# Optimization experiments

Hardware: AMD Instinct MI355X
Metric: run time of the kernel (lower is better)

The kernel has to match this reference:

```python
import jax, jax.numpy as jnp
import numpy as np

N_NODES = 50000
N_EDGES = 800000
D_NODE = 64
D_EDGE = 64
D_OUT = 64
D_HID = 128
LN_EPS = 1e-5


def _mlp_params(key, d_in):
    # layer sizes: [d_in, D_HID, D_HID, D_OUT]; weights stored [in, out]
    ks = jax.random.split(key, 3)
    dims = [d_in, D_HID, D_HID, D_OUT]
    params = []
    for i in range(3):
        s = 1.0 / np.sqrt(dims[i])
        params.append(jax.random.uniform(ks[i], (dims[i], dims[i + 1]), minval=-s, maxval=s, dtype=jnp.float32))
        params.append(jnp.zeros((dims[i + 1],), jnp.float32))
    # LayerNorm gamma/beta
    params.append(jnp.ones((D_OUT,), jnp.float32))
    params.append(jnp.zeros((D_OUT,), jnp.float32))
    return params


def _mlp_ln(h, W0, b0, W1, b1, W2, b2, g, beta):
    h = jax.nn.relu(h @ W0 + b0)
    h = jax.nn.relu(h @ W1 + b1)
    h = h @ W2 + b2
    mu = jnp.mean(h, axis=-1, keepdims=True)
    var = jnp.mean(jnp.square(h - mu), axis=-1, keepdims=True)
    return (h - mu) * jax.lax.rsqrt(var + LN_EPS) * g + beta


def setup_inputs() -> dict:
    key = jax.random.key(0)
    k = jax.random.split(key, 8)
    inp = {
        "x": jax.random.normal(k[0], (N_NODES, D_NODE), jnp.float32),
        "mesh_edge_index": jax.random.randint(k[1], (2, N_EDGES), 0, N_NODES, dtype=jnp.int32),
        "mesh_edge_attr": jax.random.normal(k[2], (N_EDGES, D_EDGE), jnp.float32),
        "world_edge_index": jax.random.randint(k[3], (2, N_EDGES), 0, N_NODES, dtype=jnp.int32),
        "world_edge_attr": jax.random.normal(k[4], (N_EDGES, D_EDGE), jnp.float32),
    }
    names = ["W0", "b0", "W1", "b1", "W2", "b2", "ln_g", "ln_b"]
    for pref, kk, d_in in [("mesh", k[5], 2 * D_NODE + D_EDGE),
                           ("world", k[6], 2 * D_NODE + D_EDGE),
                           ("upd", k[7], D_NODE + 2 * D_OUT)]:
        ps = _mlp_params(kk, d_in)
        for nm, p in zip(names, ps):
            inp[f"{pref}_{nm}"] = p
    return inp


def _edge_block(x, edge_index, edge_attr, W0, b0, W1, b1, W2, b2, g, beta):
    src, dst = edge_index[0], edge_index[1]  # PyG: x_j = source, x_i = target
    x_i = x[dst]  # [E, D_NODE]
    x_j = x[src]
    concat = jnp.concatenate([x_i, x_j, edge_attr], axis=-1)  # [E, 2D+De]
    new_edge = edge_attr + _mlp_ln(concat, W0, b0, W1, b1, W2, b2, g, beta)
    agg = jax.ops.segment_sum(new_edge, dst, num_segments=N_NODES)  # 'add' aggr at target
    return agg, new_edge


def reference(x, mesh_edge_index, mesh_edge_attr, world_edge_index, world_edge_attr,
              mesh_W0, mesh_b0, mesh_W1, mesh_b1, mesh_W2, mesh_b2, mesh_ln_g, mesh_ln_b,
              world_W0, world_b0, world_W1, world_b1, world_W2, world_b2, world_ln_g, world_ln_b,
              upd_W0, upd_b0, upd_W1, upd_b1, upd_W2, upd_b2, upd_ln_g, upd_ln_b):
    agg_m, new_edge_m = _edge_block(x, mesh_edge_index, mesh_edge_attr,
                                    mesh_W0, mesh_b0, mesh_W1, mesh_b1, mesh_W2, mesh_b2, mesh_ln_g, mesh_ln_b)
    agg_w, new_edge_w = _edge_block(x, world_edge_index, world_edge_attr,
                                    world_W0, world_b0, world_W1, world_b1, world_W2, world_b2, world_ln_g, world_ln_b)
    concat = jnp.concatenate([x, agg_m, agg_w], axis=-1)  # [N, D_NODE + 2*D_OUT]
    x_new = x + _mlp_ln(concat, upd_W0, upd_b0, upd_W1, upd_b1, upd_W2, upd_b2, upd_ln_g, upd_ln_b)
    return x_new, new_edge_m, new_edge_w
```

## Files before the change

kernel.cpp:

```cpp
#include <hip/hip_runtime.h>


#define NNODES 50000
#define NEDGES 800000
#define NBLK 512
#define NCHUNK 196

typedef __bf16 bf16x8 __attribute__((ext_vector_type(8)));
typedef float f32x4 __attribute__((ext_vector_type(4)));
#define MFMA(a, b, c) __builtin_amdgcn_mfma_f32_16x16x32_bf16(a, b, c, 0, 0, 0)

#define OFF_A 0
#define OFF_H0 24576
#define OFF_P 40960
#define OFF_PAR 43008
#define SMEM 44800

__device__ __forceinline__ unsigned short f2bf(float f) {
  unsigned u = __builtin_bit_cast(unsigned, f);
  u = (u + 0x7fffu + ((u >> 16) & 1u)) >> 16;
  return (unsigned short)u;
}
__device__ __forceinline__ unsigned long long pk4(f32x4 v) {
  union { unsigned short h[4]; unsigned long long u; } p;
  p.h[0] = f2bf(v[0]); p.h[1] = f2bf(v[1]); p.h[2] = f2bf(v[2]); p.h[3] = f2bf(v[3]);
  return p.u;
}
__device__ __forceinline__ int4 pk8(float4 a, float4 b) {
  union { unsigned short us[8]; int4 v; } u;
  u.us[0] = f2bf(a.x); u.us[1] = f2bf(a.y); u.us[2] = f2bf(a.z); u.us[3] = f2bf(a.w);
  u.us[4] = f2bf(b.x); u.us[5] = f2bf(b.y); u.us[6] = f2bf(b.z); u.us[7] = f2bf(b.w);
  return u.v;
}
__device__ __forceinline__ int4 ldpk(const float* p) {
  return pk8(*(const float4*)p, *(const float4*)(p + 4));
}

template <bool EDGE>
__global__ __launch_bounds__(512, 4) void mlp_block(
    const float* __restrict__ g1, const float* __restrict__ g2,
    const float* __restrict__ g3, const unsigned short* __restrict__ xb,
    const int* __restrict__ srcI, const int* __restrict__ dstI,
    const unsigned short* __restrict__ Wt,
    const float* __restrict__ b0, const float* __restrict__ b1,
    const float* __restrict__ b2, const float* __restrict__ gam,
    const float* __restrict__ bet, float* __restrict__ outp, int M) {
  __shared__ __align__(16) char sm[SMEM];
  const int tid = threadIdx.x, lane = tid & 63, wave = tid >> 6;
  const int lrow = lane & 15, cg = lane >> 4;
  const unsigned short* Wt0 = Wt;
  const unsigned short* Wt1 = Wt + 24576;
  const unsigned short* Wt2 = Wt + 40960;
  const int ntiles = (M + 63) >> 6;
  const int cg2 = wave & 3, rg = wave >> 2;

  for (int i = tid; i < 448; i += 512) {
    float v;
    if (i < 128) v = b0[i];
    else if (i < 256) v = b1[i - 128];
    else if (i < 320) v = b2[i - 256];
    else if (i < 384) v = gam[i - 320];
    else v = bet[i - 384];
    ((float*)(sm + OFF_PAR))[i] = v;
  }
  const float* PAR = (const float*)(sm + OFF_PAR);

  bf16x8 w0f[6], w1f[4], w2f[4];
#pragma unroll
  for (int kk = 0; kk < 6; ++kk)
    w0f[kk] = *(const bf16x8*)(Wt0 + (wave * 16 + lrow) * 192 + kk * 32 + cg * 8);
#pragma unroll
  for (int kk = 0; kk < 4; ++kk)
    w1f[kk] = *(const bf16x8*)(Wt1 + (wave * 16 + lrow) * 128 + kk * 32 + cg * 8);
#pragma unroll
  for (int kk = 0; kk < 4; ++kk)
    w2f[kk] = *(const bf16x8*)(Wt2 + (cg2 * 16 + lrow) * 128 + kk * 32 + cg * 8);

  const int srow = (tid >> 5) * 4 + ((tid & 31) >> 3), oct = tid & 7;

  int4 pxd, pxs, pat;
  auto LOADT = [&](int tt) {
    const int row = tt * 64 + srow;
    if (EDGE) {
      const int d = dstI[row], s2 = srcI[row];
      pxd = *(const int4*)(xb + (size_t)d * 64 + oct * 8);
      pxs = *(const int4*)(xb + (size_t)s2 * 64 + oct * 8);
      pat = ldpk(g3 + (size_t)row * 64 + oct * 8);
    } else {
      const int rr = min(row, M - 1);
      pxd = ldpk(g1 + (size_t)rr * 64 + oct * 8);
      pxs = ldpk(g2 + (size_t)rr * 64 + oct * 8);
      pat = ldpk(g3 + (size_t)rr * 64 + oct * 8);
    }
  };
  auto STAGE = [&]() {
    char* a0 = sm + OFF_A + srow * 384;
    const int swz = (srow & 7) << 4;
    *(int4*)(a0 + ((oct * 16) ^ swz)) = pxd;
    *(int4*)(a0 + ((128 + oct * 16) ^ swz)) = pxs;
    *(int4*)(a0 + ((256 + oct * 16) ^ swz)) = pat;
  };

  int t = blockIdx.x;
  if (t >= ntiles) return;
  LOADT(t);
  STAGE();

  for (; t < ntiles; t += NBLK) {
    const int tn = t + NBLK;
    const bool more = tn < ntiles;
    __syncthreads();
    if (more) LOADT(tn);
    {
      const f32x4 bb0 = *(const f32x4*)(PAR + wave * 16 + cg * 4);
#pragma unroll
      for (int rt = 0; rt < 4; ++rt) {
        const int row = rt * 16 + lrow, swz = (row & 7) << 4;
        const char* ab = sm + OFF_A + row * 384;
        f32x4 acc = {0.f, 0.f, 0.f, 0.f};
#pragma unroll
        for (int kk = 0; kk < 6; ++kk)
          acc = MFMA(w0f[kk], *(const bf16x8*)(ab + ((kk * 64 + cg * 16) ^ swz)), acc);
        f32x4 h;
#pragma unroll
        for (int q = 0; q < 4; ++q) h[q] = fmaxf(acc[q] + bb0[q], 0.f);
        *(unsigned long long*)(sm + OFF_H0 + row * 256 + ((wave * 32 + cg * 8) ^ swz)) = pk4(h);
      }
    }
    __syncthreads();
    {
      const f32x4 bb1 = *(const f32x4*)(PAR + 128 + wave * 16 + cg * 4);
#pragma unroll
      for (int rt = 0; rt < 4; ++rt) {
        const int row = rt * 16 + lrow, swz = (row & 7) << 4;
        const char* hb = sm + OFF_H0 + row * 256;
        f32x4 acc = {0.f, 0.f, 0.f, 0.f};
#pragma unroll
        for (int kk = 0; kk < 4; ++kk)
          acc = MFMA(w1f[kk], *(const bf16x8*)(hb + ((kk * 64 + cg * 16) ^ swz)), acc);
        f32x4 h;
#pragma unroll
        for (int q = 0; q < 4; ++q) h[q] = fmaxf(acc[q] + bb1[q], 0.f);
        *(unsigned long long*)(sm + OFF_A + row * 384 + ((wave * 32 + cg * 8) ^ swz)) = pk4(h);
      }
    }
    __syncthreads();
    f32x4 accE[2];
    {
      const f32x4 bb2 = *(const f32x4*)(PAR + 256 + cg2 * 16 + cg * 4);
#pragma unroll
      for (int j = 0; j < 2; ++j) {
        const int row = (rg * 2 + j) * 16 + lrow, swz = (row & 7) << 4;
        const char* hb = sm + OFF_A + row * 384;
        f32x4 acc = {0.f, 0.f, 0.f, 0.f};
#pragma unroll
        for (int kk = 0; kk < 4; ++kk)
          acc = MFMA(w2f[kk], *(const bf16x8*)(hb + ((kk * 64 + cg * 16) ^ swz)), acc);
#pragma unroll
        for (int q = 0; q < 4; ++q) acc[q] += bb2[q];
        float s = acc[0] + acc[1] + acc[2] + acc[3];
        float ss = acc[0] * acc[0] + acc[1] * acc[1] + acc[2] * acc[2] + acc[3] * acc[3];
        s += __shfl_xor(s, 16, 64); s += __shfl_xor(s, 32, 64);
        ss += __shfl_xor(ss, 16, 64); ss += __shfl_xor(ss, 32, 64);
        if (cg == 0) *(float2*)(sm + OFF_P + row * 32 + cg2 * 8) = make_float2(s, ss);
        accE[j] = acc;
      }
    }
    __syncthreads();
    {
      const f32x4 gv = *(const f32x4*)(PAR + 320 + cg2 * 16 + cg * 4);
      const f32x4 bv = *(const f32x4*)(PAR + 384 + cg2 * 16 + cg * 4);
#pragma unroll
      for (int j = 0; j < 2; ++j) {
        const int row = (rg * 2 + j) * 16 + lrow, gr = t * 64 + row;
        float4 p0 = *(const float4*)(sm + OFF_P + row * 32);
        float4 p1 = *(const float4*)(sm + OFF_P + row * 32 + 16);
        float s = p0.x + p0.z + p1.x + p1.z, ss = p0.y + p0.w + p1.y + p1.w;
        float mean = s * (1.f / 64.f);
        float var = fmaxf(ss * (1.f / 64.f) - mean * mean, 0.f);
        float inv = rsqrtf(var + 1e-5f);
        const int col = cg2 * 16 + cg * 4;
        const int grc = EDGE ? gr : min(gr, M - 1);
        const f32x4 r = *(const f32x4*)(g3 + (size_t)grc * 64 + col);
        f32x4 av = accE[j], o;
#pragma unroll
        for (int q = 0; q < 4; ++q) o[q] = (av[q] - mean) * inv * gv[q] + bv[q] + r[q];
        if (EDGE || gr < M) *(f32x4*)(outp + (size_t)gr * 64 + col) = o;
      }
    }
    if (more) STAGE();
  }
}

__global__ __launch_bounds__(256) void agg_k(const float* __restrict__ em,
                                             const float* __restrict__ ew,
                                             const int* __restrict__ permM,
                                             const int* __restrict__ permW,
                                             const int* __restrict__ rpM,
                                             const int* __restrict__ rpW,
                                             float* __restrict__ aggm,
                                             float* __restrict__ aggw) {
  const int lane = threadIdx.x & 63;
  const int r4 = lane >> 4, cq = lane & 15;
  const int w = (blockIdx.x * 256 + threadIdx.x) >> 6;
  const int nw = gridDim.x * 4;
  for (int dd = w; dd < 2 * NNODES; dd += nw) {
    const bool s1 = dd >= NNODES;
    const int d = s1 ? dd - NNODES : dd;
    const float* oute = s1 ? ew : em;
    const int* perm = s1 ? permW : permM;
    const int* rp = s1 ? rpW : rpM;
    const int s = rp[d], e = rp[d + 1];
    f32x4 acc = {0.f, 0.f, 0.f, 0.f}, acc2 = {0.f, 0.f, 0.f, 0.f};
    int j = s + r4;
    for (; j + 4 < e; j += 8) {
      const int ra = perm[j], rb = perm[j + 4];
      const f32x4 va = *(const f32x4*)(oute + (size_t)ra * 64 + cq * 4);
      const f32x4 vb = *(const f32x4*)(oute + (size_t)rb * 64 + cq * 4);
#pragma unroll
      for (int q = 0; q < 4; ++q) { acc[q] += va[q]; acc2[q] += vb[q]; }
    }
    if (j < e) {
      const int ra = perm[j];
      const f32x4 va = *(const f32x4*)(oute + (size_t)ra * 64 + cq * 4);
#pragma unroll
      for (int q = 0; q < 4; ++q) acc[q] += va[q];
    }
#pragma unroll
    for (int q = 0; q < 4; ++q) {
      acc[q] += acc2[q];
      acc[q] += __shfl_xor(acc[q], 16, 64);
      acc[q] += __shfl_xor(acc[q], 32, 64);
    }
    float* agg = s1 ? aggw : aggm;
    if (r4 == 0) *(f32x4*)(agg + (size_t)d * 64 + cq * 4) = acc;
  }
}

struct PrepArgs { const float* w[9]; unsigned short* wt[3]; };

__global__ void prep_w(PrepArgs pa) {
  int i = blockIdx.x * 256 + threadIdx.x;
  if (i >= 3 * 49152) return;
  int mlp = i / 49152;
  int rem = i - mlp * 49152;
  int mat, off, K, N;
  if (rem < 24576)      { mat = 0; off = 0;     K = 192; N = 128; }
  else if (rem < 40960) { mat = 1; off = 24576; K = 128; N = 128; }
  else                  { mat = 2; off = 40960; K = 128; N = 64;  }
  int local = rem - off;
  int n = local / K, k = local - n * K;
  if (mlp == 2 && mat == 0) k = (k + 64) % 192;
  pa.wt[mlp][rem] = f2bf(pa.w[mlp * 3 + mat][k * N + n]);
}

__global__ void prep_x(const float* __restrict__ x, unsigned short* __restrict__ xb) {
  int i = blockIdx.x * 256 + threadIdx.x;
  if (i < NNODES * 8) *(int4*)(xb + (size_t)i * 8) = ldpk(x + (size_t)i * 8);
}

__global__ void zero_f4(float4* p, int n) {
  int i = blockIdx.x * blockDim.x + threadIdx.x;
  if (i < n) p[i] = make_float4(0.f, 0.f, 0.f, 0.f);
}

__global__ void hist_k(const int* __restrict__ dM, const int* __restrict__ dW,
                       int* __restrict__ curM, int* __restrict__ curW, int E) {
  int i = blockIdx.x * 256 + threadIdx.x;
  if (i < E) {
    atomicAdd(curM + dM[i], 1);
    atomicAdd(curW + dW[i], 1);
  }
}

__global__ __launch_bounds__(64) void csum_k(const int* __restrict__ curM,
                                             const int* __restrict__ curW,
                                             int* __restrict__ csum) {
  const int c = blockIdx.x, set = c >= NCHUNK, c0 = c - set * NCHUNK;
  const int* cnt = set ? curW : curM;
  const int lane = threadIdx.x;
  const int base = c0 * 256 + lane * 4;
  int s = 0;
  if (base + 3 < NNODES) {
    int4 v = *(const int4*)(cnt + base);
    s = v.x + v.y + v.z + v.w;
  } else {
    for (int k = 0; k < 4; ++k) if (base + k < NNODES) s += cnt[base + k];
  }
#pragma unroll
  for (int off = 1; off < 64; off <<= 1) s += __shfl_xor(s, off, 64);
  if (lane == 0) csum[c] = s;
}

__global__ __launch_bounds__(512) void cscan_k(const int* __restrict__ csum,
                                               int* __restrict__ cbase) {
  __shared__ int buf[512];
  const int tid = threadIdx.x;
  buf[tid] = (tid < 2 * NCHUNK) ? csum[tid] : 0;
  __syncthreads();
  for (int off = 1; off < 512; off <<= 1) {
    int nv = (tid >= off) ? buf[tid - off] : 0;
    __syncthreads();
    buf[tid] += nv;
    __syncthreads();
  }
  if (tid < 2 * NCHUNK) {
    const int set = tid >= NCHUNK;
    int excl = tid ? buf[tid - 1] : 0;
    if (set) excl -= buf[NCHUNK - 1];
    cbase[tid] = excl;
  }
}

__global__ __launch_bounds__(64) void rp_k(int* __restrict__ curM, int* __restrict__ curW,
                                           const int* __restrict__ cbase,
                                           int* __restrict__ rpM, int* __restrict__ rpW) {
  const int c = blockIdx.x, set = c >= NCHUNK, c0 = c - set * NCHUNK;
  int* cnt = set ? curW : curM;
  int* rp = set ? rpW : rpM;
  const int lane = threadIdx.x;
  const int idx = c0 * 256 + lane * 4;
  int v[4];
#pragma unroll
  for (int k = 0; k < 4; ++k) v[k] = (idx + k < NNODES) ? cnt[idx + k] : 0;
  const int ls = v[0] + v[1] + v[2] + v[3];
  int ex = ls;
#pragma unroll
  for (int off = 1; off < 64; off <<= 1) {
    int nv = __shfl_up(ex, off, 64);
    if (lane >= off) ex += nv;
  }
  int run = cbase[c] + (ex - ls);
#pragma unroll
  for (int k = 0; k < 4; ++k) {
    if (idx + k < NNODES) {
      rp[idx + k] = run;
      cnt[idx + k] = run;
      run += v[k];
    }
  }
  if (c0 == 0 && lane == 0) rp[NNODES] = NEDGES;
}

__global__ void scatter_k(const int* __restrict__ dM, const int* __restrict__ dW,
                          int* __restrict__ curM, int* __restrict__ curW,
                          int* __restrict__ permM, int* __restrict__ permW, int E) {
  int i = blockIdx.x * 256 + threadIdx.x;
  if (i < E) {
    int p = atomicAdd(curM + dM[i], 1);
    permM[p] = i;
    p = atomicAdd(curW + dW[i], 1);
    permW[p] = i;
  }
}

extern "C" void kernel_launch(void* const* d_in, const int* in_sizes, int n_in,
                              void* d_out, int out_size, void* d_ws, size_t ws_size,
                              hipStream_t stream) {
  const float* x      = (const float*)d_in[0];
  const int*   meIdx  = (const int*)d_in[1];
  const float* meAttr = (const float*)d_in[2];
  const int*   weIdx  = (const int*)d_in[3];
  const float* weAttr = (const float*)d_in[4];

  float* out_x  = (float*)d_out;
  float* out_em = out_x + (size_t)NNODES * 64;
  float* out_ew = out_em + (size_t)NEDGES * 64;

  char* ws = (char*)d_ws;
  unsigned short* WtM = (unsigned short*)ws;
  unsigned short* WtW = (unsigned short*)(ws + 98304);
  unsigned short* WtU = (unsigned short*)(ws + 196608);
  unsigned short* xb  = (unsigned short*)(ws + 294912);
  float* aggm = (float*)(ws + 6694912);
  float* aggw = (float*)(ws + 19494912);
  char* p = ws + 32294912;
  int* curM  = (int*)p;
  int* curW  = curM + NNODES;
  int* rpM   = (int*)(p + 400000);
  int* rpW   = rpM + 50016;
  int* permM = rpW + 50016;
  int* permW = permM + NEDGES;
  int* csum  = permW + NEDGES;
  int* cbase = csum + 512;

  zero_f4<<<dim3(98), dim3(256), 0, stream>>>((float4*)curM, 25000);

  PrepArgs pa;
  for (int m = 0; m < 3; ++m)
    for (int l = 0; l < 3; ++l)
      pa.w[m * 3 + l] = (const float*)d_in[5 + m * 8 + l * 2];
  pa.wt[0] = WtM; pa.wt[1] = WtW; pa.wt[2] = WtU;
  prep_w<<<dim3(576), dim3(256), 0, stream>>>(pa);
  prep_x<<<dim3(1563), dim3(256), 0, stream>>>(x, xb);

  hist_k<<<dim3(3125), dim3(256), 0, stream>>>(meIdx + NEDGES, weIdx + NEDGES, curM, curW, NEDGES);
  csum_k<<<dim3(2 * NCHUNK), dim3(64), 0, stream>>>(curM, curW, csum);
  cscan_k<<<dim3(1), dim3(512), 0, stream>>>(csum, cbase);
  rp_k<<<dim3(2 * NCHUNK), dim3(64), 0, stream>>>(curM, curW, cbase, rpM, rpW);
  scatter_k<<<dim3(3125), dim3(256), 0, stream>>>(meIdx + NEDGES, weIdx + NEDGES,
                                                  curM, curW, permM, permW, NEDGES);

  mlp_block<true><<<dim3(NBLK), dim3(512), 0, stream>>>(
      nullptr, nullptr, meAttr, xb, meIdx, meIdx + NEDGES, WtM,
      (const float*)d_in[6], (const float*)d_in[8], (const float*)d_in[10],
      (const float*)d_in[11], (const float*)d_in[12],
      out_em, NEDGES);
  mlp_block<true><<<dim3(NBLK), dim3(512), 0, stream>>>(
      nullptr, nullptr, weAttr, xb, weIdx, weIdx + NEDGES, WtW,
      (const float*)d_in[14], (const float*)d_in[16], (const float*)d_in[18],
      (const float*)d_in[19], (const float*)d_in[20],
      out_ew, NEDGES);

  agg_k<<<dim3(4096), dim3(256), 0, stream>>>(out_em, out_ew, permM, permW, rpM, rpW, aggm, aggw);

  mlp_block<false><<<dim3(NBLK), dim3(512), 0, stream>>>(
      aggm, aggw, x, nullptr, nullptr, nullptr, WtU,
      (const float*)d_in[22], (const float*)d_in[24], (const float*)d_in[26],
      (const float*)d_in[27], (const float*)d_in[28],
      out_x, NNODES);
}
```

Measured before the change: 750.3 us.

## Merge mesh/world edge MLP launches and gather bf16 edge copies in aggregation

The two edge-block MLP launches become one grid of twice the blocks, with each half selecting its own edge set, weights and parameters. This removes a launch and the tail of the first kernel. When the workspace is large enough, the edge MLP also writes a bf16 copy of each new edge feature. The aggregation kernel then gathers those bf16 rows instead of fp32 rows, halving the bytes of the random gather at the cost of an extra streaming write and bf16 rounding in the segment sums.

```diff
diff --git a/kernel.cpp b/kernel.cpp
--- a/kernel.cpp
+++ b/kernel.cpp
@@ -21,6 +21,9 @@
   u = (u + 0x7fffu + ((u >> 16) & 1u)) >> 16;
   return (unsigned short)u;
 }
+__device__ __forceinline__ float bf2f(unsigned short h) {
+  return __builtin_bit_cast(float, (unsigned)h << 16);
+}
 __device__ __forceinline__ unsigned long long pk4(f32x4 v) {
   union { unsigned short h[4]; unsigned long long u; } p;
   p.h[0] = f2bf(v[0]); p.h[1] = f2bf(v[1]); p.h[2] = f2bf(v[2]); p.h[3] = f2bf(v[3]);
@@ -35,17 +38,44 @@
 __device__ __forceinline__ int4 ldpk(const float* p) {
   return pk8(*(const float4*)p, *(const float4*)(p + 4));
 }
+__device__ __forceinline__ f32x4 ub4(uint2 p) {
+  f32x4 r;
+  r[0] = bf2f((unsigned short)p.x); r[1] = bf2f((unsigned short)(p.x >> 16));
+  r[2] = bf2f((unsigned short)p.y); r[3] = bf2f((unsigned short)(p.y >> 16));
+  return r;
+}
 
 template <bool EDGE>
 __global__ __launch_bounds__(512, 4) void mlp_block(
     const float* __restrict__ g1, const float* __restrict__ g2,
-    const float* __restrict__ g3, const unsigned short* __restrict__ xb,
-    const int* __restrict__ srcI, const int* __restrict__ dstI,
-    const unsigned short* __restrict__ Wt,
-    const float* __restrict__ b0, const float* __restrict__ b1,
-    const float* __restrict__ b2, const float* __restrict__ gam,
-    const float* __restrict__ bet, float* __restrict__ outp, int M) {
+    const float* __restrict__ g3A, const float* __restrict__ g3B,
+    const unsigned short* __restrict__ xb,
+    const int* __restrict__ srcA, const int* __restrict__ dstA,
+    const int* __restrict__ srcB, const int* __restrict__ dstB,
+    const unsigned short* __restrict__ WtA,
+    const float* __restrict__ b0A, const float* __restrict__ b1A,
+    const float* __restrict__ b2A, const float* __restrict__ gmA,
+    const float* __restrict__ btA,
+    const float* __restrict__ b0B, const float* __restrict__ b1B,
+    const float* __restrict__ b2B, const float* __restrict__ gmB,
+    const float* __restrict__ btB,
+    float* __restrict__ outA, unsigned short* __restrict__ oebA, int M) {
   __shared__ __align__(16) char sm[SMEM];
+  const int gstr = EDGE ? (gridDim.x >> 1) : gridDim.x;
+  const int set = EDGE ? (int)(blockIdx.x >= (unsigned)gstr) : 0;
+  const int bid0 = blockIdx.x - set * gstr;
+  const float* g3 = set ? g3B : g3A;
+  const int* srcI = set ? srcB : srcA;
+  const int* dstI = set ? dstB : dstA;
+  const unsigned short* Wt = WtA + set * 49152;
+  const float* b0 = set ? b0B : b0A;
+  const float* b1 = set ? b1B : b1A;
+  const float* b2 = set ? b2B : b2A;
+  const float* gam = set ? gmB : gmA;
+  const float* bet = set ? btB : btA;
+  float* outp = outA + (size_t)set * NEDGES * 64;
+  unsigned short* oeb = oebA ? oebA + (size_t)set * NEDGES * 64 : nullptr;
+
   const int tid = threadIdx.x, lane = tid & 63, wave = tid >> 6;
   const int lrow = lane & 15, cg = lane >> 4;
   const unsigned short* Wt0 = Wt;
@@ -101,13 +131,13 @@
     *(int4*)(a0 + ((256 + oct * 16) ^ swz)) = pat;
   };
 
-  int t = blockIdx.x;
+  int t = bid0;
   if (t >= ntiles) return;
   LOADT(t);
   STAGE();
 
-  for (; t < ntiles; t += NBLK) {
-    const int tn = t + NBLK;
+  for (; t < ntiles; t += gstr) {
+    const int tn = t + gstr;
     const bool more = tn < ntiles;
     __syncthreads();
     if (more) LOADT(tn);
@@ -186,6 +216,7 @@
 #pragma unroll
         for (int q = 0; q < 4; ++q) o[q] = (av[q] - mean) * inv * gv[q] + bv[q] + r[q];
         if (EDGE || gr < M) *(f32x4*)(outp + (size_t)gr * 64 + col) = o;
+        if (EDGE && oeb) *(unsigned long long*)(oeb + (size_t)gr * 64 + col) = pk4(o);
       }
     }
     if (more) STAGE();
@@ -194,6 +225,7 @@
 
 __global__ __launch_bounds__(256) void agg_k(const float* __restrict__ em,
                                              const float* __restrict__ ew,
+                                             const unsigned short* __restrict__ oeb,
                                              const int* __restrict__ permM,
                                              const int* __restrict__ permW,
                                              const int* __restrict__ rpM,
@@ -207,24 +239,39 @@
   for (int dd = w; dd < 2 * NNODES; dd += nw) {
     const bool s1 = dd >= NNODES;
     const int d = s1 ? dd - NNODES : dd;
-    const float* oute = s1 ? ew : em;
     const int* perm = s1 ? permW : permM;
     const int* rp = s1 ? rpW : rpM;
     const int s = rp[d], e = rp[d + 1];
     f32x4 acc = {0.f, 0.f, 0.f, 0.f}, acc2 = {0.f, 0.f, 0.f, 0.f};
     int j = s + r4;
-    for (; j + 4 < e; j += 8) {
-      const int ra = perm[j], rb = perm[j + 4];
-      const f32x4 va = *(const f32x4*)(oute + (size_t)ra * 64 + cq * 4);
-      const f32x4 vb = *(const f32x4*)(oute + (size_t)rb * 64 + cq * 4);
-#pragma unroll
-      for (int q = 0; q < 4; ++q) { acc[q] += va[q]; acc2[q] += vb[q]; }
-    }
-    if (j < e) {
-      const int ra = perm[j];
-      const f32x4 va = *(const f32x4*)(oute + (size_t)ra * 64 + cq * 4);
-#pragma unroll
-      for (int q = 0; q < 4; ++q) acc[q] += va[q];
+    if (oeb) {
+      const unsigned short* ob = oeb + (size_t)(s1 ? NEDGES : 0) * 64;
+      for (; j + 4 < e; j += 8) {
+        const int ra = perm[j], rb = perm[j + 4];
+        const f32x4 va = ub4(*(const uint2*)(ob + (size_t)ra * 64 + cq * 4));
+        const f32x4 vb = ub4(*(const uint2*)(ob + (size_t)rb * 64 + cq * 4));
+#pragma unroll
+        for (int q = 0; q < 4; ++q) { acc[q] += va[q]; acc2[q] += vb[q]; }
+      }
+      if (j < e) {
+        const f32x4 va = ub4(*(const uint2*)(ob + (size_t)perm[j] * 64 + cq * 4));
+#pragma unroll
+        for (int q = 0; q < 4; ++q) acc[q] += va[q];
+      }
+    } else {
+      const float* oute = s1 ? ew : em;
+      for (; j + 4 < e; j += 8) {
+        const int ra = perm[j], rb = perm[j + 4];
+        const f32x4 va = *(const f32x4*)(oute + (size_t)ra * 64 + cq * 4);
+        const f32x4 vb = *(const f32x4*)(oute + (size_t)rb * 64 + cq * 4);
+#pragma unroll
+        for (int q = 0; q < 4; ++q) { acc[q] += va[q]; acc2[q] += vb[q]; }
+      }
+      if (j < e) {
+        const f32x4 va = *(const f32x4*)(oute + (size_t)perm[j] * 64 + cq * 4);
+#pragma unroll
+        for (int q = 0; q < 4; ++q) acc[q] += va[q];
+      }
     }
 #pragma unroll
     for (int q = 0; q < 4; ++q) {
@@ -369,7 +416,6 @@
 
   char* ws = (char*)d_ws;
   unsigned short* WtM = (unsigned short*)ws;
-  unsigned short* WtW = (unsigned short*)(ws + 98304);
   unsigned short* WtU = (unsigned short*)(ws + 196608);
   unsigned short* xb  = (unsigned short*)(ws + 294912);
   float* aggm = (float*)(ws + 6694912);
@@ -383,6 +429,10 @@
   int* permW = permM + NEDGES;
   int* csum  = permW + NEDGES;
   int* cbase = csum + 512;
+  char* pend = (char*)(cbase + 512);
+  const size_t oeb_bytes = (size_t)2 * NEDGES * 64 * 2;
+  unsigned short* oeb =
+      (ws_size >= (size_t)(pend - ws) + oeb_bytes) ? (unsigned short*)pend : nullptr;
 
   zero_f4<<<dim3(98), dim3(256), 0, stream>>>((float4*)curM, 25000);
 
@@ -390,7 +440,7 @@
   for (int m = 0; m < 3; ++m)
     for (int l = 0; l < 3; ++l)
       pa.w[m * 3 + l] = (const float*)d_in[5 + m * 8 + l * 2];
-  pa.wt[0] = WtM; pa.wt[1] = WtW; pa.wt[2] = WtU;
+  pa.wt[0] = WtM; pa.wt[1] = WtM + 49152; pa.wt[2] = WtU;
   prep_w<<<dim3(576), dim3(256), 0, stream>>>(pa);
   prep_x<<<dim3(1563), dim3(256), 0, stream>>>(x, xb);
 
@@ -401,22 +451,23 @@
   scatter_k<<<dim3(3125), dim3(256), 0, stream>>>(meIdx + NEDGES, weIdx + NEDGES,
                                                   curM, curW, permM, permW, NEDGES);
 
-  mlp_block<true><<<dim3(NBLK), dim3(512), 0, stream>>>(
-      nullptr, nullptr, meAttr, xb, meIdx, meIdx + NEDGES, WtM,
+  mlp_block<true><<<dim3(2 * NBLK), dim3(512), 0, stream>>>(
+      nullptr, nullptr, meAttr, weAttr, xb,
+      meIdx, meIdx + NEDGES, weIdx, weIdx + NEDGES, WtM,
       (const float*)d_in[6], (const float*)d_in[8], (const float*)d_in[10],
       (const float*)d_in[11], (const float*)d_in[12],
-      out_em, NEDGES);
-  mlp_block<true><<<dim3(NBLK), dim3(512), 0, stream>>>(
-      nullptr, nullptr, weAttr, xb, weIdx, weIdx + NEDGES, WtW,
       (const float*)d_in[14], (const float*)d_in[16], (const float*)d_in[18],
       (const float*)d_in[19], (const float*)d_in[20],
-      out_ew, NEDGES);
-
-  agg_k<<<dim3(4096), dim3(256), 0, stream>>>(out_em, out_ew, permM, permW, rpM, rpW, aggm, aggw);
+      out_em, oeb, NEDGES);
+
+  agg_k<<<dim3(4096), dim3(256), 0, stream>>>(out_em, out_ew, oeb,
+                                              permM, permW, rpM, rpW, aggm, aggw);
 
   mlp_block<false><<<dim3(NBLK), dim3(512), 0, stream>>>(
-      aggm, aggw, x, nullptr, nullptr, nullptr, WtU,
+      aggm, aggw, x, nullptr, xb,
+      nullptr, nullptr, nullptr, nullptr, WtU,
       (const float*)d_in[22], (const float*)d_in[24], (const float*)d_in[26],
       (const float*)d_in[27], (const float*)d_in[28],
-      out_x, NNODES);
-}
+      nullptr, nullptr, nullptr, nullptr, nullptr,
+      out_x, nullptr, NNODES);
+}
```

Measured after the change: 887.9 us. 1.18x slower.

## Process edges in destination-sorted order and aggregate from a contiguous bf16 copy

Applied to the files above, without the earlier changes.

The scatter kernel now also writes destination-sorted src and dst index arrays, and the edge MLP iterates edges in that sorted order. It gathers edge_attr and writes the fp32 output through the permutation. When the workspace is large enough, the edge kernel also writes a bf16 copy of each new edge row in sorted order. The aggregation kernel then streams that copy contiguously instead of doing permuted fp32 gathers. This trades scattered attr reads and output writes plus an extra bf16 store for contiguous aggregation reads and better node-feature locality, and adds bf16 rounding to the aggregated sums.

```diff
diff --git a/kernel.cpp b/kernel.cpp
--- a/kernel.cpp
+++ b/kernel.cpp
@@ -21,6 +21,9 @@
   u = (u + 0x7fffu + ((u >> 16) & 1u)) >> 16;
   return (unsigned short)u;
 }
+__device__ __forceinline__ float bf2f(unsigned short h) {
+  return __builtin_bit_cast(float, (unsigned)h << 16);
+}
 __device__ __forceinline__ unsigned long long pk4(f32x4 v) {
   union { unsigned short h[4]; unsigned long long u; } p;
   p.h[0] = f2bf(v[0]); p.h[1] = f2bf(v[1]); p.h[2] = f2bf(v[2]); p.h[3] = f2bf(v[3]);
@@ -35,16 +38,23 @@
 __device__ __forceinline__ int4 ldpk(const float* p) {
   return pk8(*(const float4*)p, *(const float4*)(p + 4));
 }
+__device__ __forceinline__ f32x4 ub4(uint2 p) {
+  f32x4 r;
+  r[0] = bf2f((unsigned short)p.x); r[1] = bf2f((unsigned short)(p.x >> 16));
+  r[2] = bf2f((unsigned short)p.y); r[3] = bf2f((unsigned short)(p.y >> 16));
+  return r;
+}
 
 template <bool EDGE>
 __global__ __launch_bounds__(512, 4) void mlp_block(
     const float* __restrict__ g1, const float* __restrict__ g2,
     const float* __restrict__ g3, const unsigned short* __restrict__ xb,
-    const int* __restrict__ srcI, const int* __restrict__ dstI,
-    const unsigned short* __restrict__ Wt,
+    const int* __restrict__ srcS, const int* __restrict__ dstS,
+    const int* __restrict__ perm, const unsigned short* __restrict__ Wt,
     const float* __restrict__ b0, const float* __restrict__ b1,
     const float* __restrict__ b2, const float* __restrict__ gam,
-    const float* __restrict__ bet, float* __restrict__ outp, int M) {
+    const float* __restrict__ bet, float* __restrict__ outp,
+    unsigned short* __restrict__ oebS, int M) {
   __shared__ __align__(16) char sm[SMEM];
   const int tid = threadIdx.x, lane = tid & 63, wave = tid >> 6;
   const int lrow = lane & 15, cg = lane >> 4;
@@ -82,10 +92,10 @@
   auto LOADT = [&](int tt) {
     const int row = tt * 64 + srow;
     if (EDGE) {
-      const int d = dstI[row], s2 = srcI[row];
+      const int d = dstS[row], s2 = srcS[row], e = perm[row];
       pxd = *(const int4*)(xb + (size_t)d * 64 + oct * 8);
       pxs = *(const int4*)(xb + (size_t)s2 * 64 + oct * 8);
-      pat = ldpk(g3 + (size_t)row * 64 + oct * 8);
+      pat = ldpk(g3 + (size_t)e * 64 + oct * 8);
     } else {
       const int rr = min(row, M - 1);
       pxd = ldpk(g1 + (size_t)rr * 64 + oct * 8);
@@ -180,12 +190,22 @@
         float var = fmaxf(ss * (1.f / 64.f) - mean * mean, 0.f);
         float inv = rsqrtf(var + 1e-5f);
         const int col = cg2 * 16 + cg * 4;
-        const int grc = EDGE ? gr : min(gr, M - 1);
-        const f32x4 r = *(const f32x4*)(g3 + (size_t)grc * 64 + col);
-        f32x4 av = accE[j], o;
-#pragma unroll
-        for (int q = 0; q < 4; ++q) o[q] = (av[q] - mean) * inv * gv[q] + bv[q] + r[q];
-        if (EDGE || gr < M) *(f32x4*)(outp + (size_t)gr * 64 + col) = o;
+        if (EDGE) {
+          const int pm = perm[gr];
+          const f32x4 r = *(const f32x4*)(g3 + (size_t)pm * 64 + col);
+          f32x4 av = accE[j], o;
+#pragma unroll
+          for (int q = 0; q < 4; ++q) o[q] = (av[q] - mean) * inv * gv[q] + bv[q] + r[q];
+          *(f32x4*)(outp + (size_t)pm * 64 + col) = o;
+          if (oebS) *(unsigned long long*)(oebS + (size_t)gr * 64 + col) = pk4(o);
+        } else {
+          const int grc = min(gr, M - 1);
+          const f32x4 r = *(const f32x4*)(g3 + (size_t)grc * 64 + col);
+          f32x4 av = accE[j], o;
+#pragma unroll
+          for (int q = 0; q < 4; ++q) o[q] = (av[q] - mean) * inv * gv[q] + bv[q] + r[q];
+          if (gr < M) *(f32x4*)(outp + (size_t)gr * 64 + col) = o;
+        }
       }
     }
     if (more) STAGE();
@@ -194,6 +214,7 @@
 
 __global__ __launch_bounds__(256) void agg_k(const float* __restrict__ em,
                                              const float* __restrict__ ew,
+                                             const unsigned short* __restrict__ oebS,
                                              const int* __restrict__ permM,
                                              const int* __restrict__ permW,
                                              const int* __restrict__ rpM,
@@ -207,24 +228,38 @@
   for (int dd = w; dd < 2 * NNODES; dd += nw) {
     const bool s1 = dd >= NNODES;
     const int d = s1 ? dd - NNODES : dd;
-    const float* oute = s1 ? ew : em;
-    const int* perm = s1 ? permW : permM;
     const int* rp = s1 ? rpW : rpM;
     const int s = rp[d], e = rp[d + 1];
     f32x4 acc = {0.f, 0.f, 0.f, 0.f}, acc2 = {0.f, 0.f, 0.f, 0.f};
     int j = s + r4;
-    for (; j + 4 < e; j += 8) {
-      const int ra = perm[j], rb = perm[j + 4];
-      const f32x4 va = *(const f32x4*)(oute + (size_t)ra * 64 + cq * 4);
-      const f32x4 vb = *(const f32x4*)(oute + (size_t)rb * 64 + cq * 4);
-#pragma unroll
-      for (int q = 0; q < 4; ++q) { acc[q] += va[q]; acc2[q] += vb[q]; }
-    }
-    if (j < e) {
-      const int ra = perm[j];
-      const f32x4 va = *(const f32x4*)(oute + (size_t)ra * 64 + cq * 4);
-#pragma unroll
-      for (int q = 0; q < 4; ++q) acc[q] += va[q];
+    if (oebS) {
+      const unsigned short* ob = oebS + (size_t)(s1 ? NEDGES : 0) * 64;
+      for (; j + 4 < e; j += 8) {
+        const f32x4 va = ub4(*(const uint2*)(ob + (size_t)j * 64 + cq * 4));
+        const f32x4 vb = ub4(*(const uint2*)(ob + (size_t)(j + 4) * 64 + cq * 4));
+#pragma unroll
+        for (int q = 0; q < 4; ++q) { acc[q] += va[q]; acc2[q] += vb[q]; }
+      }
+      if (j < e) {
+        const f32x4 va = ub4(*(const uint2*)(ob + (size_t)j * 64 + cq * 4));
+#pragma unroll
+        for (int q = 0; q < 4; ++q) acc[q] += va[q];
+      }
+    } else {
+      const float* oute = s1 ? ew : em;
+      const int* perm = s1 ? permW : permM;
+      for (; j + 4 < e; j += 8) {
+        const int ra = perm[j], rb = perm[j + 4];
+        const f32x4 va = *(const f32x4*)(oute + (size_t)ra * 64 + cq * 4);
+        const f32x4 vb = *(const f32x4*)(oute + (size_t)rb * 64 + cq * 4);
+#pragma unroll
+        for (int q = 0; q < 4; ++q) { acc[q] += va[q]; acc2[q] += vb[q]; }
+      }
+      if (j < e) {
+        const f32x4 va = *(const f32x4*)(oute + (size_t)perm[j] * 64 + cq * 4);
+#pragma unroll
+        for (int q = 0; q < 4; ++q) acc[q] += va[q];
+      }
     }
 #pragma unroll
     for (int q = 0; q < 4; ++q) {
@@ -343,14 +378,19 @@
 }
 
 __global__ void scatter_k(const int* __restrict__ dM, const int* __restrict__ dW,
+                          const int* __restrict__ sM, const int* __restrict__ sW,
                           int* __restrict__ curM, int* __restrict__ curW,
-                          int* __restrict__ permM, int* __restrict__ permW, int E) {
+                          int* __restrict__ permM, int* __restrict__ permW,
+                          int* __restrict__ dstSM, int* __restrict__ dstSW,
+                          int* __restrict__ srcSM, int* __restrict__ srcSW, int E) {
   int i = blockIdx.x * 256 + threadIdx.x;
   if (i < E) {
-    int p = atomicAdd(curM + dM[i], 1);
-    permM[p] = i;
-    p = atomicAdd(curW + dW[i], 1);
-    permW[p] = i;
+    int d = dM[i];
+    int p = atomicAdd(curM + d, 1);
+    permM[p] = i; dstSM[p] = d; srcSM[p] = sM[i];
+    d = dW[i];
+    p = atomicAdd(curW + d, 1);
+    permW[p] = i; dstSW[p] = d; srcSW[p] = sW[i];
   }
 }
 
@@ -381,8 +421,16 @@
   int* rpW   = rpM + 50016;
   int* permM = rpW + 50016;
   int* permW = permM + NEDGES;
-  int* csum  = permW + NEDGES;
+  int* dstSM = permW + NEDGES;
+  int* dstSW = dstSM + NEDGES;
+  int* srcSM = dstSW + NEDGES;
+  int* srcSW = srcSM + NEDGES;
+  int* csum  = srcSW + NEDGES;
   int* cbase = csum + 512;
+  char* pend = (char*)(cbase + 512);
+  const size_t oeb_bytes = (size_t)2 * NEDGES * 64 * 2;
+  unsigned short* oebS =
+      (ws_size >= (size_t)(pend - ws) + oeb_bytes) ? (unsigned short*)pend : nullptr;
 
   zero_f4<<<dim3(98), dim3(256), 0, stream>>>((float4*)curM, 25000);
 
@@ -399,24 +447,27 @@
   cscan_k<<<dim3(1), dim3(512), 0, stream>>>(csum, cbase);
   rp_k<<<dim3(2 * NCHUNK), dim3(64), 0, stream>>>(curM, curW, cbase, rpM, rpW);
   scatter_k<<<dim3(3125), dim3(256), 0, stream>>>(meIdx + NEDGES, weIdx + NEDGES,
-                                                  curM, curW, permM, permW, NEDGES);
+                                                  meIdx, weIdx, curM, curW,
+                                                  permM, permW, dstSM, dstSW,
+                                                  srcSM, srcSW, NEDGES);
 
   mlp_block<true><<<dim3(NBLK), dim3(512), 0, stream>>>(
-      nullptr, nullptr, meAttr, xb, meIdx, meIdx + NEDGES, WtM,
+      nullptr, nullptr, meAttr, xb, srcSM, dstSM, permM, WtM,
       (const float*)d_in[6], (const float*)d_in[8], (const float*)d_in[10],
       (const float*)d_in[11], (const float*)d_in[12],
-      out_em, NEDGES);
+      out_em, oebS, NEDGES);
   mlp_block<true><<<dim3(NBLK), dim3(512), 0, stream>>>(
-      nullptr, nullptr, weAttr, xb, weIdx, weIdx + NEDGES, WtW,
+      nullptr, nullptr, weAttr, xb, srcSW, dstSW, permW, WtW,
       (const float*)d_in[14], (const float*)d_in[16], (const float*)d_in[18],
       (const float*)d_in[19], (const float*)d_in[20],
-      out_ew, NEDGES);
-
-  agg_k<<<dim3(4096), dim3(256), 0, stream>>>(out_em, out_ew, permM, permW, rpM, rpW, aggm, aggw);
+      out_ew, oebS ? oebS + (size_t)NEDGES * 64 : nullptr, NEDGES);
+
+  agg_k<<<dim3(4096), dim3(256), 0, stream>>>(out_em, out_ew, oebS,
+                                              permM, permW, rpM, rpW, aggm, aggw);
 
   mlp_block<false><<<dim3(NBLK), dim3(512), 0, stream>>>(
-      aggm, aggw, x, nullptr, nullptr, nullptr, WtU,
+      aggm, aggw, x, nullptr, nullptr, nullptr, nullptr, WtU,
       (const float*)d_in[22], (const float*)d_in[24], (const float*)d_in[26],
       (const float*)d_in[27], (const float*)d_in[28],
-      out_x, NNODES);
-}
+      out_x, nullptr, NNODES);
+}
```

Result: slower. 826.5 us (+10.2%).

## Fuse CSR edge aggregation into node update MLP kernel

Applied to the files above, without the earlier changes.

Removes the separate aggregation kernel and its fp32 aggm/aggw round trip through global memory. A new node_mlp kernel gathers each node's incoming mesh and world edge rows via the CSR permutation, sums them in registers, packs them to bf16 in shared memory, and runs the update MLP and LayerNorm directly. The grid is 782 blocks, one 64-row tile each, so the gather for a tile is serialized per thread (8 floats per thread, one row per 8 threads). The tile's MFMA work cannot start until its gather finishes, and the gather has less parallelism than the old agg_k.

```diff
diff --git a/kernel.cpp b/kernel.cpp
--- a/kernel.cpp
+++ b/kernel.cpp
@@ -34,6 +34,9 @@
 }
 __device__ __forceinline__ int4 ldpk(const float* p) {
   return pk8(*(const float4*)p, *(const float4*)(p + 4));
+}
+__device__ __forceinline__ void add4(float4& a, float4 v) {
+  a.x += v.x; a.y += v.y; a.z += v.z; a.w += v.w;
 }
 
 template <bool EDGE>
@@ -192,48 +195,166 @@
   }
 }
 
-__global__ __launch_bounds__(256) void agg_k(const float* __restrict__ em,
-                                             const float* __restrict__ ew,
-                                             const int* __restrict__ permM,
-                                             const int* __restrict__ permW,
-                                             const int* __restrict__ rpM,
-                                             const int* __restrict__ rpW,
-                                             float* __restrict__ aggm,
-                                             float* __restrict__ aggw) {
-  const int lane = threadIdx.x & 63;
-  const int r4 = lane >> 4, cq = lane & 15;
-  const int w = (blockIdx.x * 256 + threadIdx.x) >> 6;
-  const int nw = gridDim.x * 4;
-  for (int dd = w; dd < 2 * NNODES; dd += nw) {
-    const bool s1 = dd >= NNODES;
-    const int d = s1 ? dd - NNODES : dd;
-    const float* oute = s1 ? ew : em;
-    const int* perm = s1 ? permW : permM;
-    const int* rp = s1 ? rpW : rpM;
-    const int s = rp[d], e = rp[d + 1];
-    f32x4 acc = {0.f, 0.f, 0.f, 0.f}, acc2 = {0.f, 0.f, 0.f, 0.f};
-    int j = s + r4;
-    for (; j + 4 < e; j += 8) {
-      const int ra = perm[j], rb = perm[j + 4];
-      const f32x4 va = *(const f32x4*)(oute + (size_t)ra * 64 + cq * 4);
-      const f32x4 vb = *(const f32x4*)(oute + (size_t)rb * 64 + cq * 4);
-#pragma unroll
-      for (int q = 0; q < 4; ++q) { acc[q] += va[q]; acc2[q] += vb[q]; }
-    }
-    if (j < e) {
-      const int ra = perm[j];
-      const f32x4 va = *(const f32x4*)(oute + (size_t)ra * 64 + cq * 4);
-#pragma unroll
-      for (int q = 0; q < 4; ++q) acc[q] += va[q];
-    }
-#pragma unroll
-    for (int q = 0; q < 4; ++q) {
-      acc[q] += acc2[q];
-      acc[q] += __shfl_xor(acc[q], 16, 64);
-      acc[q] += __shfl_xor(acc[q], 32, 64);
-    }
-    float* agg = s1 ? aggw : aggm;
-    if (r4 == 0) *(f32x4*)(agg + (size_t)d * 64 + cq * 4) = acc;
+__global__ __launch_bounds__(512, 4) void node_mlp(
+    const float* __restrict__ xg, const float* __restrict__ em,
+    const float* __restrict__ ew, const int* __restrict__ permM,
+    const int* __restrict__ permW, const int* __restrict__ rpM,
+    const int* __restrict__ rpW, const unsigned short* __restrict__ Wt,
+    const float* __restrict__ b0, const float* __restrict__ b1,
+    const float* __restrict__ b2, const float* __restrict__ gam,
+    const float* __restrict__ bet, float* __restrict__ outp, int M) {
+  __shared__ __align__(16) char sm[SMEM];
+  const int tid = threadIdx.x, lane = tid & 63, wave = tid >> 6;
+  const int lrow = lane & 15, cg = lane >> 4;
+  const unsigned short* Wt0 = Wt;
+  const unsigned short* Wt1 = Wt + 24576;
+  const unsigned short* Wt2 = Wt + 40960;
+  const int ntiles = (M + 63) >> 6;
+  const int cg2 = wave & 3, rg = wave >> 2;
+
+  for (int i = tid; i < 448; i += 512) {
+    float v;
+    if (i < 128) v = b0[i];
+    else if (i < 256) v = b1[i - 128];
+    else if (i < 320) v = b2[i - 256];
+    else if (i < 384) v = gam[i - 320];
+    else v = bet[i - 384];
+    ((float*)(sm + OFF_PAR))[i] = v;
+  }
+  const float* PAR = (const float*)(sm + OFF_PAR);
+
+  bf16x8 w0f[6], w1f[4], w2f[4];
+#pragma unroll
+  for (int kk = 0; kk < 6; ++kk)
+    w0f[kk] = *(const bf16x8*)(Wt0 + (wave * 16 + lrow) * 192 + kk * 32 + cg * 8);
+#pragma unroll
+  for (int kk = 0; kk < 4; ++kk)
+    w1f[kk] = *(const bf16x8*)(Wt1 + (wave * 16 + lrow) * 128 + kk * 32 + cg * 8);
+#pragma unroll
+  for (int kk = 0; kk < 4; ++kk)
+    w2f[kk] = *(const bf16x8*)(Wt2 + (cg2 * 16 + lrow) * 128 + kk * 32 + cg * 8);
+
+  const int srow = (tid >> 5) * 4 + ((tid & 31) >> 3), oct = tid & 7;
+
+  for (int t = blockIdx.x; t < ntiles; t += gridDim.x) {
+    {
+      const int gr = t * 64 + srow;
+      const int rr = min(gr, M - 1);
+      const int4 px = ldpk(xg + (size_t)rr * 64 + oct * 8);
+      float4 am0 = {0.f, 0.f, 0.f, 0.f}, am1 = {0.f, 0.f, 0.f, 0.f};
+      float4 aw0 = {0.f, 0.f, 0.f, 0.f}, aw1 = {0.f, 0.f, 0.f, 0.f};
+      if (gr < M) {
+        int j = rpM[gr];
+        const int e = rpM[gr + 1];
+        for (; j + 1 < e; j += 2) {
+          const int pa = permM[j], pb = permM[j + 1];
+          const float* ra = em + (size_t)pa * 64 + oct * 8;
+          const float* rb = em + (size_t)pb * 64 + oct * 8;
+          add4(am0, *(const float4*)ra); add4(am1, *(const float4*)(ra + 4));
+          add4(am0, *(const float4*)rb); add4(am1, *(const float4*)(rb + 4));
+        }
+        if (j < e) {
+          const float* ra = em + (size_t)permM[j] * 64 + oct * 8;
+          add4(am0, *(const float4*)ra); add4(am1, *(const float4*)(ra + 4));
+        }
+        j = rpW[gr];
+        const int e2 = rpW[gr + 1];
+        for (; j + 1 < e2; j += 2) {
+          const int pa = permW[j], pb = permW[j + 1];
+          const float* ra = ew + (size_t)pa * 64 + oct * 8;
+          const float* rb = ew + (size_t)pb * 64 + oct * 8;
+          add4(aw0, *(const float4*)ra); add4(aw1, *(const float4*)(ra + 4));
+          add4(aw0, *(const float4*)rb); add4(aw1, *(const float4*)(rb + 4));
+        }
+        if (j < e2) {
+          const float* ra = ew + (size_t)permW[j] * 64 + oct * 8;
+          add4(aw0, *(const float4*)ra); add4(aw1, *(const float4*)(ra + 4));
+        }
+      }
+      char* a0 = sm + OFF_A + srow * 384;
+      const int swz = (srow & 7) << 4;
+      *(int4*)(a0 + ((oct * 16) ^ swz)) = pk8(am0, am1);
+      *(int4*)(a0 + ((128 + oct * 16) ^ swz)) = pk8(aw0, aw1);
+      *(int4*)(a0 + ((256 + oct * 16) ^ swz)) = px;
+    }
+    __syncthreads();
+    {
+      const f32x4 bb0 = *(const f32x4*)(PAR + wave * 16 + cg * 4);
+#pragma unroll
+      for (int rt = 0; rt < 4; ++rt) {
+        const int row = rt * 16 + lrow, swz = (row & 7) << 4;
+        const char* ab = sm + OFF_A + row * 384;
+        f32x4 acc = {0.f, 0.f, 0.f, 0.f};
+#pragma unroll
+        for (int kk = 0; kk < 6; ++kk)
+          acc = MFMA(w0f[kk], *(const bf16x8*)(ab + ((kk * 64 + cg * 16) ^ swz)), acc);
+        f32x4 h;
+#pragma unroll
+        for (int q = 0; q < 4; ++q) h[q] = fmaxf(acc[q] + bb0[q], 0.f);
+        *(unsigned long long*)(sm + OFF_H0 + row * 256 + ((wave * 32 + cg * 8) ^ swz)) = pk4(h);
+      }
+    }
+    __syncthreads();
+    {
+      const f32x4 bb1 = *(const f32x4*)(PAR + 128 + wave * 16 + cg * 4);
+#pragma unroll
+      for (int rt = 0; rt < 4; ++rt) {
+        const int row = rt * 16 + lrow, swz = (row & 7) << 4;
+        const char* hb = sm + OFF_H0 + row * 256;
+        f32x4 acc = {0.f, 0.f, 0.f, 0.f};
+#pragma unroll
+        for (int kk = 0; kk < 4; ++kk)
+          acc = MFMA(w1f[kk], *(const bf16x8*)(hb + ((kk * 64 + cg * 16) ^ swz)), acc);
+        f32x4 h;
+#pragma unroll
+        for (int q = 0; q < 4; ++q) h[q] = fmaxf(acc[q] + bb1[q], 0.f);
+        *(unsigned long long*)(sm + OFF_A + row * 384 + ((wave * 32 + cg * 8) ^ swz)) = pk4(h);
+      }
+    }
+    __syncthreads();
+    f32x4 accE[2];
+    {
+      const f32x4 bb2 = *(const f32x4*)(PAR + 256 + cg2 * 16 + cg * 4);
+#pragma unroll
+      for (int j = 0; j < 2; ++j) {
+        const int row = (rg * 2 + j) * 16 + lrow, swz = (row & 7) << 4;
+        const char* hb = sm + OFF_A + row * 384;
+        f32x4 acc = {0.f, 0.f, 0.f, 0.f};
+#pragma unroll
+        for (int kk = 0; kk < 4; ++kk)
+          acc = MFMA(w2f[kk], *(const bf16x8*)(hb + ((kk * 64 + cg * 16) ^ swz)), acc);
+#pragma unroll
+        for (int q = 0; q < 4; ++q) acc[q] += bb2[q];
+        float s = acc[0] + acc[1] + acc[2] + acc[3];
+        float ss = acc[0] * acc[0] + acc[1] * acc[1] + acc[2] * acc[2] + acc[3] * acc[3];
+        s += __shfl_xor(s, 16, 64); s += __shfl_xor(s, 32, 64);
+        ss += __shfl_xor(ss, 16, 64); ss += __shfl_xor(ss, 32, 64);
+        if (cg == 0) *(float2*)(sm + OFF_P + row * 32 + cg2 * 8) = make_float2(s, ss);
+        accE[j] = acc;
+      }
+    }
+    __syncthreads();
+    {
+      const f32x4 gv = *(const f32x4*)(PAR + 320 + cg2 * 16 + cg * 4);
+      const f32x4 bv = *(const f32x4*)(PAR + 384 + cg2 * 16 + cg * 4);
+#pragma unroll
+      for (int j = 0; j < 2; ++j) {
+        const int row = (rg * 2 + j) * 16 + lrow, gr = t * 64 + row;
+        float4 p0 = *(const float4*)(sm + OFF_P + row * 32);
+        float4 p1 = *(const float4*)(sm + OFF_P + row * 32 + 16);
+        float s = p0.x + p0.z + p1.x + p1.z, ss = p0.y + p0.w + p1.y + p1.w;
+        float mean = s * (1.f / 64.f);
+        float var = fmaxf(ss * (1.f / 64.f) - mean * mean, 0.f);
+        float inv = rsqrtf(var + 1e-5f);
+        const int col = cg2 * 16 + cg * 4;
+        const int grc = min(gr, M - 1);
+        const f32x4 r = *(const f32x4*)(xg + (size_t)grc * 64 + col);
+        f32x4 av = accE[j], o;
+#pragma unroll
+        for (int q = 0; q < 4; ++q) o[q] = (av[q] - mean) * inv * gv[q] + bv[q] + r[q];
+        if (gr < M) *(f32x4*)(outp + (size_t)gr * 64 + col) = o;
+      }
+    }
   }
 }
 
@@ -372,8 +493,6 @@
   unsigned short* WtW = (unsigned short*)(ws + 98304);
   unsigned short* WtU = (unsigned short*)(ws + 196608);
   unsigned short* xb  = (unsigned short*)(ws + 294912);
-  float* aggm = (float*)(ws + 6694912);
-  float* aggw = (float*)(ws + 19494912);
   char* p = ws + 32294912;
   int* curM  = (int*)p;
   int* curW  = curM + NNODES;
@@ -412,10 +531,8 @@
       (const float*)d_in[19], (const float*)d_in[20],
       out_ew, NEDGES);
 
-  agg_k<<<dim3(4096), dim3(256), 0, stream>>>(out_em, out_ew, permM, permW, rpM, rpW, aggm, aggw);
-
-  mlp_block<false><<<dim3(NBLK), dim3(512), 0, stream>>>(
-      aggm, aggw, x, nullptr, nullptr, nullptr, WtU,
+  node_mlp<<<dim3(782), dim3(512), 0, stream>>>(
+      x, out_em, out_ew, permM, permW, rpM, rpW, WtU,
       (const float*)d_in[22], (const float*)d_in[24], (const float*)d_in[26],
       (const float*)d_in[27], (const float*)d_in[28],
       out_x, NNODES);
```

After: 762.3 us. No clear change (+1.6%).
